# Optimization experiments

Measured on AMD Instinct MI355X. Metric: run time of the kernel, lower is better.

Reference implementation:

```python
import math
import jax, jax.numpy as jnp
import numpy as np

B, T, C, H = 2, 2048, 1024, 16
MAX_SEQ = 2048


def _make_pe(max_seq: int, dim: int, base: float = 10000.0) -> np.ndarray:
    pe = np.zeros((max_seq, dim), dtype=np.float32)
    position = np.arange(max_seq, dtype=np.float32)[:, None]
    div_term = np.exp(np.arange(0, dim, 2, dtype=np.float32) * (-math.log(base) / dim))
    pe[:, 0::2] = np.sin(position * div_term)
    pe[:, 1::2] = np.cos(position * div_term)
    return pe


def setup_inputs() -> dict:
    key = jax.random.key(0)
    k1, k2, k3 = jax.random.split(key, 3)
    x = jax.random.normal(k1, (B, T, C), dtype=jnp.float32)
    # torch Linear default init scale ~ 1/sqrt(fan_in)
    w_qkv = jax.random.normal(k2, (3 * C, C), dtype=jnp.float32) / math.sqrt(C)
    w_proj = jax.random.normal(k3, (C, C), dtype=jnp.float32) / math.sqrt(C)
    pe = jnp.asarray(_make_pe(MAX_SEQ, C))
    return {"x": x, "w_qkv": w_qkv, "w_proj": w_proj, "pe": pe}


def reference(x, w_qkv, w_proj, pe):
    b, t, c = x.shape
    h = H
    d = c // h
    # RoPE module adds sinusoidal PE under torch.no_grad() -> stop_gradient
    xp = jax.lax.stop_gradient(x + pe[None, :t, :])
    qkv = xp @ w_qkv.T  # [b, t, 3c]
    q, k, v = jnp.split(qkv, 3, axis=-1)
    q = q.reshape(b, t, h, d).transpose(0, 2, 1, 3)  # bhtd
    k = k.reshape(b, t, h, d).transpose(0, 2, 1, 3)
    v = v.reshape(b, t, h, d).transpose(0, 2, 1, 3)
    att = jnp.einsum("bhqd,bhkd->bhqk", q, k) * (1.0 / math.sqrt(d))
    causal = jnp.tril(jnp.ones((t, t), dtype=bool))  # [t, t]
    att = jnp.where(causal[None, None], att, -jnp.inf)
    att = jax.nn.softmax(att, axis=-1)
    y = jnp.einsum("bhqk,bhkd->bhqd", att, v)
    y = y.transpose(0, 2, 1, 3).reshape(b, t, c)
    return y @ w_proj.T
```

## Files before the change

kernel.cpp:

```cpp
#include <hip/hip_runtime.h>
#include <cstdint>

typedef __bf16 bf16x8 __attribute__((ext_vector_type(8)));
typedef __bf16 bf16x4 __attribute__((ext_vector_type(4)));
typedef float  f32x4  __attribute__((ext_vector_type(4)));

static constexpr int kB = 2, kT = 2048, kC = 1024, kH = 16, kD = 64;
static constexpr int kK = 1024;

__device__ __forceinline__ uint16_t f2bf(float f) {
  uint32_t u = __builtin_bit_cast(uint32_t, f);
  u += 0x7FFFu + ((u >> 16) & 1u);
  return (uint16_t)(u >> 16);
}

__device__ __forceinline__ void gl_lds16(const void* g, void* l) {
  __builtin_amdgcn_global_load_lds((__attribute__((address_space(1))) void*)(void*)g,
                                   (__attribute__((address_space(3))) void*)l, 16, 0, 0);
}

__device__ const uint8_t kJT[48] = {
    95, 127, 94, 15, 126, 93, 125, 92, 14, 124, 91, 123, 90, 13, 122, 89,
    121, 88, 12, 120, 87, 119, 86, 11, 118, 85, 117, 84, 10, 116, 83, 115,
    82, 9, 114, 81, 113, 80, 8, 112, 7, 6, 5, 4, 3, 2, 1, 0};

__global__ __launch_bounds__(256) void prep_all(const float* __restrict__ x,
                                                const float* __restrict__ pe,
                                                const float* __restrict__ wqkv,
                                                const float* __restrict__ wproj,
                                                uint16_t* __restrict__ xp,
                                                uint16_t* __restrict__ wq,
                                                uint16_t* __restrict__ wp) {
  constexpr int NX = kB * kT * kC / 4;
  constexpr int NWQ = 3 * kC * kC / 4;
  const int i = blockIdx.x * 256 + threadIdx.x;
  if (i < NX) {
    const float4 xv = ((const float4*)x)[i];
    const int c4 = i & (kC / 4 - 1);
    const int t = (i / (kC / 4)) & (kT - 1);
    const float4 pv = ((const float4*)pe)[t * (kC / 4) + c4];
    ushort4 o;
    o.x = f2bf(xv.x + pv.x);
    o.y = f2bf(xv.y + pv.y);
    o.z = f2bf(xv.z + pv.z);
    o.w = f2bf(xv.w + pv.w);
    ((ushort4*)xp)[i] = o;
  } else if (i < NX + NWQ) {
    const int j = i - NX;
    const float4 v = ((const float4*)wqkv)[j];
    ushort4 u;
    u.x = f2bf(v.x); u.y = f2bf(v.y); u.z = f2bf(v.z); u.w = f2bf(v.w);
    ((ushort4*)wq)[j] = u;
  } else {
    const int j = i - NX - NWQ;
    const float4 v = ((const float4*)wproj)[j];
    ushort4 u;
    u.x = f2bf(v.x); u.y = f2bf(v.y); u.z = f2bf(v.z); u.w = f2bf(v.w);
    ((ushort4*)wp)[j] = u;
  }
}

__global__ __launch_bounds__(512, 2) void gemm_qkv(const uint16_t* __restrict__ A,
                                                   const uint16_t* __restrict__ W,
                                                   uint16_t* __restrict__ qb,
                                                   uint16_t* __restrict__ kb,
                                                   uint16_t* __restrict__ vT) {
  __shared__ __align__(1024) char lds[131072];
  const int tid = threadIdx.x;
  const int lane = tid & 63;
  const int wid = tid >> 6;
  const int l15 = lane & 15, l4 = lane >> 4;
  const int WM = wid >> 2, WN = wid & 3;
  const int orig = (int)blockIdx.x;
  const int xcd = orig & 7, j = orig >> 3;
  const int m0 = (xcd * 2 + (j & 1)) * 256;
  const int n0 = (j >> 1) * 256;

  f32x4 acc[2][4][4] = {};
  bf16x8 bfp[2][4];

  auto stage = [&](int isA, int buf, int kt) {
#pragma unroll
    for (int c = 0; c < 4; ++c) {
      const int off = (c * 512 + tid) * 16;
      const int lr = off >> 7, cbl = off & 127;
      const size_t grow = (size_t)((isA ? m0 : n0) + lr) * kK + kt * 64;
      gl_lds16((const char*)(isA ? A : W) + grow * 2 + (cbl ^ ((lr & 7) << 4)),
               lds + (isA ? 0 : 65536) + buf * 32768 + off);
    }
  };

#define QKV_PHASE(CBUF, H, SA, SBUF, KT, VM)                                      \
  {                                                                               \
    stage(SA, SBUF, KT);                                                          \
    if (VM == 4)                                                                  \
      asm volatile("s_waitcnt vmcnt(4)" ::: "memory");                            \
    else                                                                          \
      asm volatile("s_waitcnt vmcnt(8)" ::: "memory");                            \
    __builtin_amdgcn_s_barrier();                                                 \
    asm volatile("" ::: "memory");                                                \
    const char* Ab = lds + (CBUF)*32768;                                          \
    const char* Bb = lds + 65536 + (CBUF)*32768;                                  \
    if ((H) == 0) {                                                               \
      _Pragma("unroll") for (int ks = 0; ks < 2; ++ks)                            \
          _Pragma("unroll") for (int nt = 0; nt < 4; ++nt) {                      \
        const int lr = WN * 64 + nt * 16 + l15;                                   \
        bfp[ks][nt] = *(const bf16x8*)(Bb + lr * 128 +                            \
                                       ((ks * 64 + l4 * 16) ^ ((lr & 7) << 4)));  \
      }                                                                           \
    }                                                                             \
    _Pragma("unroll") for (int ks = 0; ks < 2; ++ks) {                            \
      bf16x8 af[4];                                                               \
      _Pragma("unroll") for (int mt = 0; mt < 4; ++mt) {                          \
        const int lr = (H)*128 + WM * 64 + mt * 16 + l15;                         \
        af[mt] = *(const bf16x8*)(Ab + lr * 128 +                                 \
                                  ((ks * 64 + l4 * 16) ^ ((lr & 7) << 4)));       \
      }                                                                           \
      __builtin_amdgcn_s_setprio(1);                                              \
      _Pragma("unroll") for (int mt = 0; mt < 4; ++mt)                            \
          _Pragma("unroll") for (int nt = 0; nt < 4; ++nt)                        \
              acc[H][mt][nt] = __builtin_amdgcn_mfma_f32_16x16x32_bf16(           \
                  af[mt], bfp[ks][nt], acc[H][mt][nt], 0, 0, 0);                  \
      __builtin_amdgcn_s_setprio(0);                                              \
    }                                                                             \
    asm volatile("" ::: "memory");                                                \
    __builtin_amdgcn_s_barrier();                                                 \
    asm volatile("" ::: "memory");                                                \
  }

  stage(1, 0, 0);
  stage(0, 0, 0);

  for (int i = 0; i < 8; ++i) {
    const int ktb1 = 2 * i + 1;
    const int ktb0 = (2 * i + 2 > 15) ? 15 : 2 * i + 2;
    QKV_PHASE(0, 0, 1, 1, ktb1, 4);
    QKV_PHASE(0, 1, 0, 1, ktb1, 8);
    QKV_PHASE(1, 0, 1, 0, ktb0, 4);
    QKV_PHASE(1, 1, 0, 0, ktb0, 8);
  }
  asm volatile("s_waitcnt vmcnt(0)" ::: "memory");
  __builtin_amdgcn_s_barrier();
  asm volatile("" ::: "memory");

  const int sec = n0 >> 10;
  const int b = m0 >> 11, tb = m0 & (kT - 1);
  if (sec < 2) {
    uint16_t* dst = (sec == 0) ? qb : kb;
#pragma unroll
    for (int h = 0; h < 2; ++h)
#pragma unroll
      for (int mt = 0; mt < 4; ++mt)
#pragma unroll
        for (int nt = 0; nt < 4; ++nt)
#pragma unroll
          for (int r = 0; r < 4; ++r) {
            const int m = h * 128 + WM * 64 + mt * 16 + l4 * 4 + r;
            const int nn = (n0 & (kC - 1)) + WN * 64 + nt * 16 + l15;
            const int hh = nn >> 6, d = nn & 63;
            dst[((size_t)((b * kH + hh) * kT + tb + m)) * kD + d] =
                f2bf(acc[h][mt][nt][r]);
          }
  } else {
#pragma unroll
    for (int h = 0; h < 2; ++h)
#pragma unroll
      for (int mt = 0; mt < 4; ++mt)
#pragma unroll
        for (int nt = 0; nt < 4; ++nt) {
          const int nl = WN * 64 + nt * 16 + l15;
          const int mb2 = (h * 128 + WM * 64 + mt * 16 + l4 * 4) * 2;
          ushort4 pk;
          pk.x = f2bf(acc[h][mt][nt][0]);
          pk.y = f2bf(acc[h][mt][nt][1]);
          pk.z = f2bf(acc[h][mt][nt][2]);
          pk.w = f2bf(acc[h][mt][nt][3]);
          *(ushort4*)(lds + nl * 512 + (mb2 ^ ((nl & 7) << 4))) = pk;
        }
    asm volatile("" ::: "memory");
    __builtin_amdgcn_s_barrier();
    asm volatile("" ::: "memory");
#pragma unroll
    for (int it = 0; it < 16; ++it) {
      const int chunk = it * 512 + tid;
      const int nr = chunk >> 5, mb = (chunk & 31) * 16;
      const bf16x8 v = *(const bf16x8*)(lds + nr * 512 + (mb ^ ((nr & 7) << 4)));
      const int nn = (n0 - 2048) + nr;
      const int hh = nn >> 6, d = nn & 63;
      *(bf16x8*)(vT + ((size_t)((b * kH + hh) * kD + d)) * kT + tb + (chunk & 31) * 8) = v;
    }
  }
#undef QKV_PHASE
}

__global__ __launch_bounds__(256, 2) void gemm_proj(const uint16_t* __restrict__ A,
                                                    const uint16_t* __restrict__ W,
                                                    float* __restrict__ out) {
  __shared__ __align__(1024) char lds[65536];
  const int tid = threadIdx.x;
  const int lane = tid & 63;
  const int wid = tid >> 6;
  const int l15 = lane & 15, l4 = lane >> 4;
  const int WM = wid >> 1, WN = wid & 1;
  const int orig = (int)blockIdx.x;
  const int xcd = orig & 7, j = orig >> 3;
  const int m0 = (xcd * 4 + (j & 3)) * 128;
  const int n0 = (j >> 2) * 128;

  f32x4 acc[2][2][4] = {};
  bf16x8 bfp[2][4];

  auto stage = [&](int isA, int buf, int kt) {
#pragma unroll
    for (int c = 0; c < 4; ++c) {
      const int off = (c * 256 + tid) * 16;
      const int lr = off >> 7, cbl = off & 127;
      const size_t grow = (size_t)((isA ? m0 : n0) + lr) * kK + kt * 64;
      gl_lds16((const char*)(isA ? A : W) + grow * 2 + (cbl ^ ((lr & 7) << 4)),
               lds + (isA ? 0 : 32768) + buf * 16384 + off);
    }
  };

#define PRJ_PHASE(CBUF, H, SA, SBUF, KT, VM)                                      \
  {                                                                               \
    stage(SA, SBUF, KT);                                                          \
    if (VM == 4)                                                                  \
      asm volatile("s_waitcnt vmcnt(4)" ::: "memory");                            \
    else                                                                          \
      asm volatile("s_waitcnt vmcnt(8)" ::: "memory");                            \
    __builtin_amdgcn_s_barrier();                                                 \
    asm volatile("" ::: "memory");                                                \
    const char* Ab = lds + (CBUF)*16384;                                          \
    const char* Bb = lds + 32768 + (CBUF)*16384;                                  \
    if ((H) == 0) {                                                               \
      _Pragma("unroll") for (int ks = 0; ks < 2; ++ks)                            \
          _Pragma("unroll") for (int nt = 0; nt < 4; ++nt) {                      \
        const int lr = WN * 64 + nt * 16 + l15;                                   \
        bfp[ks][nt] = *(const bf16x8*)(Bb + lr * 128 +                            \
                                       ((ks * 64 + l4 * 16) ^ ((lr & 7) << 4)));  \
      }                                                                           \
    }                                                                             \
    _Pragma("unroll") for (int ks = 0; ks < 2; ++ks) {                            \
      bf16x8 af[2];                                                               \
      _Pragma("unroll") for (int mt = 0; mt < 2; ++mt) {                          \
        const int lr = (H)*64 + WM * 32 + mt * 16 + l15;                          \
        af[mt] = *(const bf16x8*)(Ab + lr * 128 +                                 \
                                  ((ks * 64 + l4 * 16) ^ ((lr & 7) << 4)));       \
      }                                                                           \
      __builtin_amdgcn_s_setprio(1);                                              \
      _Pragma("unroll") for (int mt = 0; mt < 2; ++mt)                            \
          _Pragma("unroll") for (int nt = 0; nt < 4; ++nt)                        \
              acc[H][mt][nt] = __builtin_amdgcn_mfma_f32_16x16x32_bf16(           \
                  af[mt], bfp[ks][nt], acc[H][mt][nt], 0, 0, 0);                  \
      __builtin_amdgcn_s_setprio(0);                                              \
    }                                                                             \
    asm volatile("" ::: "memory");                                                \
    __builtin_amdgcn_s_barrier();                                                 \
    asm volatile("" ::: "memory");                                                \
  }

  stage(1, 0, 0);
  stage(0, 0, 0);

  for (int i = 0; i < 8; ++i) {
    const int ktb1 = 2 * i + 1;
    const int ktb0 = (2 * i + 2 > 15) ? 15 : 2 * i + 2;
    PRJ_PHASE(0, 0, 1, 1, ktb1, 4);
    PRJ_PHASE(0, 1, 0, 1, ktb1, 8);
    PRJ_PHASE(1, 0, 1, 0, ktb0, 4);
    PRJ_PHASE(1, 1, 0, 0, ktb0, 8);
  }
  asm volatile("s_waitcnt vmcnt(0)" ::: "memory");
  __builtin_amdgcn_s_barrier();
  asm volatile("" ::: "memory");

#pragma unroll
  for (int h = 0; h < 2; ++h)
#pragma unroll
    for (int mt = 0; mt < 2; ++mt)
#pragma unroll
      for (int nt = 0; nt < 4; ++nt)
#pragma unroll
        for (int r = 0; r < 4; ++r) {
          const int m = m0 + h * 64 + WM * 32 + mt * 16 + l4 * 4 + r;
          const int n = n0 + WN * 64 + nt * 16 + l15;
          out[(size_t)m * kC + n] = acc[h][mt][nt][r];
        }
#undef PRJ_PHASE
}

__global__ __launch_bounds__(256, 4) void attn(const uint16_t* __restrict__ qb,
                                               const uint16_t* __restrict__ kb,
                                               const uint16_t* __restrict__ vT,
                                               uint16_t* __restrict__ y,
                                               uint16_t* __restrict__ opart,
                                               float* __restrict__ ml) {
  __shared__ __align__(1024) char lds[40960];
  const int lane = threadIdx.x & 63;
  const int wid = threadIdx.x >> 6;
  const int l15 = lane & 15, l4 = lane >> 4;
  const int bh = blockIdx.x;
  const int enc = kJT[blockIdx.y];
  const int qt = enc & 31, half = (enc >> 5) & 1, split = enc >> 6;
  const int nkt = qt + 1;
  const int h0 = (nkt + 1) >> 1;
  const int lo = (split && half) ? h0 : 0;
  const int hi = split ? (half ? nkt : h0) : nkt;
  const int q0 = qt * 64 + wid * 16;
  const size_t base = (size_t)bh * kT * kD;
  const uint16_t* Q = qb + base;
  const uint16_t* Kp = kb + base;
  const uint16_t* Vt = vT + base;
  char* P = lds + 32768 + wid * 2048;
  const int xr = (l15 & 7) << 4;

  bf16x8 qf[2];
#pragma unroll
  for (int ks = 0; ks < 2; ++ks) {
    bf16x8 t = *(const bf16x8*)(Q + (size_t)(q0 + l15) * kD + ks * 32 + l4 * 8);
#pragma unroll
    for (int i = 0; i < 8; ++i) t[i] = (__bf16)((float)t[i] * 0.1803368801f);
    qf[ks] = t;
  }
  bf16x8 ones;
#pragma unroll
  for (int i = 0; i < 8; ++i) ones[i] = (__bf16)1.0f;

  float m_ = -1e30f;
  f32x4 o[4];
  f32x4 ol = {0.f, 0.f, 0.f, 0.f};
#pragma unroll
  for (int nt = 0; nt < 4; ++nt) o[nt] = (f32x4){0.f, 0.f, 0.f, 0.f};

  auto STAGE = [&](int bi, int k0) {
#pragma unroll
    for (int c = 0; c < 2; ++c) {
      const int call = wid * 2 + c;
      const int row = call * 8 + (lane >> 3);
      const int colb = (((lane & 7) ^ ((lane >> 3) & 7)) << 4);
      gl_lds16((const char*)Kp + ((size_t)(k0 + row) * kD) * 2 + colb,
               lds + bi * 8192 + call * 1024);
      gl_lds16((const char*)Vt + ((size_t)row * kT + k0) * 2 + colb,
               lds + 16384 + bi * 8192 + call * 1024);
    }
  };

  int cur = 0;
  STAGE(0, lo * 64);
  for (int kt = lo; kt < hi; ++kt) {
    const int k0 = kt * 64;
    asm volatile("s_waitcnt vmcnt(0)" ::: "memory");
    __builtin_amdgcn_s_barrier();
    asm volatile("" ::: "memory");
    if (kt + 1 < hi) STAGE(cur ^ 1, k0 + 64);

    const char* Kb = lds + cur * 8192;
    const char* Vb = lds + 16384 + cur * 8192;

    f32x4 s[4] = {};
    __builtin_amdgcn_s_setprio(1);
#pragma unroll
    for (int ks = 0; ks < 2; ++ks)
#pragma unroll
      for (int nt = 0; nt < 4; ++nt) {
        const bf16x8 kf =
            *(const bf16x8*)(Kb + (nt * 16 + l15) * 128 + ((ks * 64 + l4 * 16) ^ xr));
        s[nt] = __builtin_amdgcn_mfma_f32_16x16x32_bf16(kf, qf[ks], s[nt], 0, 0, 0);
      }
    __builtin_amdgcn_s_setprio(0);

    if (kt == nkt - 1) {
      const int qq = q0 + l15;
#pragma unroll
      for (int nt = 0; nt < 4; ++nt)
#pragma unroll
        for (int r = 0; r < 4; ++r)
          if (k0 + nt * 16 + l4 * 4 + r > qq) s[nt][r] = -1e30f;
    }

    float tmx[4];
#pragma unroll
    for (int nt = 0; nt < 4; ++nt)
      tmx[nt] = fmaxf(fmaxf(fmaxf(s[nt][0], s[nt][1]), s[nt][2]), s[nt][3]);
    const float pm = fmaxf(fmaxf(fmaxf(tmx[0], tmx[1]), tmx[2]), tmx[3]);
    if (!__all(pm <= m_ + 11.0f)) {
      float rm = fmaxf(pm, __shfl_xor(pm, 16));
      rm = fmaxf(rm, __shfl_xor(rm, 32));
      const float newm = fmaxf(m_, rm);
      const float sc = exp2f(m_ - newm);
      m_ = newm;
#pragma unroll
      for (int nt = 0; nt < 4; ++nt)
#pragma unroll
        for (int r = 0; r < 4; ++r) o[nt][r] *= sc;
#pragma unroll
      for (int r = 0; r < 4; ++r) ol[r] *= sc;
    }
#pragma unroll
    for (int nt = 0; nt < 4; ++nt)
#pragma unroll
      for (int r = 0; r < 4; ++r) s[nt][r] = exp2f(s[nt][r] - m_);

#pragma unroll
    for (int nt = 0; nt < 4; ++nt) {
      bf16x4 pk;
#pragma unroll
      for (int r = 0; r < 4; ++r) pk[r] = (__bf16)s[nt][r];
      *(bf16x4*)(P + l15 * 128 + ((nt * 32 + l4 * 8) ^ xr)) = pk;
    }
    asm volatile("s_waitcnt lgkmcnt(0)" ::: "memory");
    __builtin_amdgcn_sched_barrier(0);

    bf16x8 pf[2];
#pragma unroll
    for (int ks = 0; ks < 2; ++ks)
      pf[ks] = *(const bf16x8*)(P + l15 * 128 + ((ks * 64 + l4 * 16) ^ xr));
    __builtin_amdgcn_s_setprio(1);
#pragma unroll
    for (int ks = 0; ks < 2; ++ks) {
#pragma unroll
      for (int nt = 0; nt < 4; ++nt) {
        const bf16x8 vf =
            *(const bf16x8*)(Vb + (nt * 16 + l15) * 128 + ((ks * 64 + l4 * 16) ^ xr));
        o[nt] = __builtin_amdgcn_mfma_f32_16x16x32_bf16(vf, pf[ks], o[nt], 0, 0, 0);
      }
      ol = __builtin_amdgcn_mfma_f32_16x16x32_bf16(ones, pf[ks], ol, 0, 0, 0);
    }
    __builtin_amdgcn_s_setprio(0);

    cur ^= 1;
  }

  if (!split) {
    const float inv = 1.0f / ol[0];
    const int b = bh >> 4, h = bh & 15;
    const int q = q0 + l15;
#pragma unroll
    for (int nt = 0; nt < 4; ++nt) {
      bf16x4 yv;
#pragma unroll
      for (int r = 0; r < 4; ++r) yv[r] = (__bf16)(o[nt][r] * inv);
      *(bf16x4*)(y + ((size_t)(b * kT + q)) * kC + h * kD + nt * 16 + l4 * 4) = yv;
    }
  } else {
    const int prow = (qt - 16) * 64 + wid * 16 + l15;
    uint16_t* op = opart + (((size_t)(half * 32 + bh)) * 1024 + prow) * 64;
#pragma unroll
    for (int nt = 0; nt < 4; ++nt) {
      bf16x4 ov;
#pragma unroll
      for (int r = 0; r < 4; ++r) ov[r] = (__bf16)o[nt][r];
      *(bf16x4*)(op + nt * 16 + l4 * 4) = ov;
    }
    if (l4 == 0) {
      float* mlp = ml + (((size_t)(half * 32 + bh)) * 1024 + prow) * 2;
      mlp[0] = m_;
      mlp[1] = ol[0];
    }
  }
}

__global__ __launch_bounds__(256) void attn_combine(const uint16_t* __restrict__ op,
                                                    const float* __restrict__ ml,
                                                    uint16_t* __restrict__ y) {
  const int gid = blockIdx.x * 256 + threadIdx.x;
  const int r = gid >> 3, c8 = (gid & 7) * 8;
  const int bh = r >> 10, row = r & 1023;
  const float m0 = ml[((size_t)(bh * 1024 + row)) * 2];
  const float l0 = ml[((size_t)(bh * 1024 + row)) * 2 + 1];
  const float m1 = ml[((size_t)((32 + bh) * 1024 + row)) * 2];
  const float l1 = ml[((size_t)((32 + bh) * 1024 + row)) * 2 + 1];
  const float M = fmaxf(m0, m1);
  const float w0 = exp2f(m0 - M), w1 = exp2f(m1 - M);
  const float inv = 1.0f / (l0 * w0 + l1 * w1);
  const bf16x8 a = *(const bf16x8*)(op + ((size_t)(bh * 1024 + row)) * 64 + c8);
  const bf16x8 bvec = *(const bf16x8*)(op + ((size_t)((32 + bh) * 1024 + row)) * 64 + c8);
  const int b = bh >> 4, h = bh & 15;
  const int t = (16 + (row >> 6)) * 64 + (row & 63);
  bf16x8 out;
#pragma unroll
  for (int j = 0; j < 8; ++j)
    out[j] = (__bf16)(((float)a[j] * w0 + (float)bvec[j] * w1) * inv);
  *(bf16x8*)(y + ((size_t)(b * kT + t)) * kC + h * kD + c8) = out;
}

extern "C" void kernel_launch(void* const* d_in, const int* in_sizes, int n_in,
                              void* d_out, int out_size, void* d_ws, size_t ws_size,
                              hipStream_t stream) {
  const float* x = (const float*)d_in[0];
  const float* wqkv = (const float*)d_in[1];
  const float* wproj = (const float*)d_in[2];
  const float* pe = (const float*)d_in[3];

  char* ws = (char*)d_ws;
  uint16_t* xp = (uint16_t*)(ws);
  uint16_t* wq = (uint16_t*)(ws + (size_t)(8u << 20));
  uint16_t* wp = (uint16_t*)(ws + (size_t)(14u << 20));
  uint16_t* qbuf = (uint16_t*)(ws + (size_t)(16u << 20));
  uint16_t* kbuf = (uint16_t*)(ws + (size_t)(24u << 20));
  uint16_t* vTb = (uint16_t*)(ws + (size_t)(32u << 20));
  uint16_t* opart = (uint16_t*)(ws + (size_t)(40u << 20));
  float* mlb = (float*)(ws + (size_t)(48u << 20));

  prep_all<<<dim3(8192), 256, 0, stream>>>(x, pe, wqkv, wproj, xp, wq, wp);

  gemm_qkv<<<dim3(192), 512, 0, stream>>>(xp, wq, qbuf, kbuf, vTb);

  attn<<<dim3(kB * kH, 48), 256, 0, stream>>>(qbuf, kbuf, vTb, xp, opart, mlb);
  attn_combine<<<dim3(1024), 256, 0, stream>>>(opart, mlb, xp);

  gemm_proj<<<dim3(256), 256, 0, stream>>>(xp, wp, (float*)d_out);
}
```

Measured before the change: 102.1 us.

## Split attention KV ranges into up to four chunks by query tile depth

Replaces the two-way split-K scheme for the upper half of query tiles with a graded split: tiles 24-31 use four KV chunks, 16-23 three, 8-15 two, and the rest one. The grid grows from 48 to 80 blocks per head, and the combine kernel now merges up to four partials for rows from query tile 8 onward. The aim is to even out per-block work and give the GPU more parallel blocks, so the long causal tiles no longer dominate the tail. In exchange, more partial outputs go through global memory and the combine kernel handles more rows.

```diff
diff --git a/kernel.cpp b/kernel.cpp
--- a/kernel.cpp
+++ b/kernel.cpp
@@ -18,11 +18,6 @@
   __builtin_amdgcn_global_load_lds((__attribute__((address_space(1))) void*)(void*)g,
                                    (__attribute__((address_space(3))) void*)l, 16, 0, 0);
 }
-
-__device__ const uint8_t kJT[48] = {
-    95, 127, 94, 15, 126, 93, 125, 92, 14, 124, 91, 123, 90, 13, 122, 89,
-    121, 88, 12, 120, 87, 119, 86, 11, 118, 85, 117, 84, 10, 116, 83, 115,
-    82, 9, 114, 81, 113, 80, 8, 112, 7, 6, 5, 4, 3, 2, 1, 0};
 
 __global__ __launch_bounds__(256) void prep_all(const float* __restrict__ x,
                                                 const float* __restrict__ pe,
@@ -300,12 +295,18 @@
   const int wid = threadIdx.x >> 6;
   const int l15 = lane & 15, l4 = lane >> 4;
   const int bh = blockIdx.x;
-  const int enc = kJT[blockIdx.y];
-  const int qt = enc & 31, half = (enc >> 5) & 1, split = enc >> 6;
+  const int jy = (int)blockIdx.y;
+  int qt, c;
+  if (jy < 32) { qt = 31 - (jy >> 2); c = jy & 3; }
+  else if (jy < 56) { const int t = jy - 32; qt = 23 - t / 3; c = t % 3; }
+  else if (jy < 72) { const int t = jy - 56; qt = 15 - ((t) >> 1); c = t & 1; }
+  else { qt = 7 - (jy - 72); c = 0; }
   const int nkt = qt + 1;
-  const int h0 = (nkt + 1) >> 1;
-  const int lo = (split && half) ? h0 : 0;
-  const int hi = split ? (half ? nkt : h0) : nkt;
+  const int nch = (qt >= 24) ? 4 : (qt >= 16) ? 3 : (qt >= 8) ? 2 : 1;
+  const int bas = nkt / nch, rem = nkt % nch;
+  const int lo = c * bas + (c < rem ? c : rem);
+  const int hi = lo + bas + (c < rem ? 1 : 0);
+  const int split = (nch > 1);
   const int q0 = qt * 64 + wid * 16;
   const size_t base = (size_t)bh * kT * kD;
   const uint16_t* Q = qb + base;
@@ -334,8 +335,8 @@
 
   auto STAGE = [&](int bi, int k0) {
 #pragma unroll
-    for (int c = 0; c < 2; ++c) {
-      const int call = wid * 2 + c;
+    for (int cc = 0; cc < 2; ++cc) {
+      const int call = wid * 2 + cc;
       const int row = call * 8 + (lane >> 3);
       const int colb = (((lane & 7) ^ ((lane >> 3) & 7)) << 4);
       gl_lds16((const char*)Kp + ((size_t)(k0 + row) * kD) * 2 + colb,
@@ -443,8 +444,11 @@
       *(bf16x4*)(y + ((size_t)(b * kT + q)) * kC + h * kD + nt * 16 + l4 * 4) = yv;
     }
   } else {
-    const int prow = (qt - 16) * 64 + wid * 16 + l15;
-    uint16_t* op = opart + (((size_t)(half * 32 + bh)) * 1024 + prow) * 64;
+    const int slot = (qt >= 24) ? ((qt - 24) * 4 + c)
+                   : (qt >= 16) ? (32 + (qt - 16) * 3 + c)
+                                : (56 + (qt - 8) * 2 + c);
+    const int row64 = wid * 16 + l15;
+    uint16_t* op = opart + (((size_t)(bh * 72 + slot)) * 64 + row64) * 64;
 #pragma unroll
     for (int nt = 0; nt < 4; ++nt) {
       bf16x4 ov;
@@ -453,7 +457,7 @@
       *(bf16x4*)(op + nt * 16 + l4 * 4) = ov;
     }
     if (l4 == 0) {
-      float* mlp = ml + (((size_t)(half * 32 + bh)) * 1024 + prow) * 2;
+      float* mlp = ml + (((size_t)(bh * 72 + slot)) * 64 + row64) * 2;
       mlp[0] = m_;
       mlp[1] = ol[0];
     }
@@ -465,22 +469,47 @@
                                                     uint16_t* __restrict__ y) {
   const int gid = blockIdx.x * 256 + threadIdx.x;
   const int r = gid >> 3, c8 = (gid & 7) * 8;
-  const int bh = r >> 10, row = r & 1023;
-  const float m0 = ml[((size_t)(bh * 1024 + row)) * 2];
-  const float l0 = ml[((size_t)(bh * 1024 + row)) * 2 + 1];
-  const float m1 = ml[((size_t)((32 + bh) * 1024 + row)) * 2];
-  const float l1 = ml[((size_t)((32 + bh) * 1024 + row)) * 2 + 1];
-  const float M = fmaxf(m0, m1);
-  const float w0 = exp2f(m0 - M), w1 = exp2f(m1 - M);
-  const float inv = 1.0f / (l0 * w0 + l1 * w1);
-  const bf16x8 a = *(const bf16x8*)(op + ((size_t)(bh * 1024 + row)) * 64 + c8);
-  const bf16x8 bvec = *(const bf16x8*)(op + ((size_t)((32 + bh) * 1024 + row)) * 64 + c8);
+  const int bh = r / 1536, rowg = r % 1536;
+  const int qt = 8 + (rowg >> 6), row64 = rowg & 63;
+  int s0, nch;
+  if (qt >= 24) { s0 = (qt - 24) * 4; nch = 4; }
+  else if (qt >= 16) { s0 = 32 + (qt - 16) * 3; nch = 3; }
+  else { s0 = 56 + (qt - 8) * 2; nch = 2; }
+  float mv[4], lv[4];
+#pragma unroll
+  for (int i = 0; i < 4; ++i) {
+    if (i < nch) {
+      const size_t mi = (((size_t)(bh * 72 + s0 + i)) * 64 + row64) * 2;
+      mv[i] = ml[mi];
+      lv[i] = ml[mi + 1];
+    } else {
+      mv[i] = -1e30f;
+      lv[i] = 0.f;
+    }
+  }
+  const float M = fmaxf(fmaxf(mv[0], mv[1]), fmaxf(mv[2], mv[3]));
+  float w[4], L = 0.f;
+#pragma unroll
+  for (int i = 0; i < 4; ++i) {
+    w[i] = exp2f(mv[i] - M);
+    L += lv[i] * w[i];
+  }
+  float acc[8] = {};
+#pragma unroll
+  for (int i = 0; i < 4; ++i) {
+    if (i < nch) {
+      const bf16x8 ov =
+          *(const bf16x8*)(op + (((size_t)(bh * 72 + s0 + i)) * 64 + row64) * 64 + c8);
+#pragma unroll
+      for (int jj = 0; jj < 8; ++jj) acc[jj] += (float)ov[jj] * w[i];
+    }
+  }
+  const float inv = 1.0f / L;
   const int b = bh >> 4, h = bh & 15;
-  const int t = (16 + (row >> 6)) * 64 + (row & 63);
+  const int t = 512 + rowg;
   bf16x8 out;
 #pragma unroll
-  for (int j = 0; j < 8; ++j)
-    out[j] = (__bf16)(((float)a[j] * w0 + (float)bvec[j] * w1) * inv);
+  for (int jj = 0; jj < 8; ++jj) out[jj] = (__bf16)(acc[jj] * inv);
   *(bf16x8*)(y + ((size_t)(b * kT + t)) * kC + h * kD + c8) = out;
 }
 
@@ -500,14 +529,14 @@
   uint16_t* kbuf = (uint16_t*)(ws + (size_t)(24u << 20));
   uint16_t* vTb = (uint16_t*)(ws + (size_t)(32u << 20));
   uint16_t* opart = (uint16_t*)(ws + (size_t)(40u << 20));
-  float* mlb = (float*)(ws + (size_t)(48u << 20));
+  float* mlb = (float*)(ws + (size_t)(60u << 20));
 
   prep_all<<<dim3(8192), 256, 0, stream>>>(x, pe, wqkv, wproj, xp, wq, wp);
 
   gemm_qkv<<<dim3(192), 512, 0, stream>>>(xp, wq, qbuf, kbuf, vTb);
 
-  attn<<<dim3(kB * kH, 48), 256, 0, stream>>>(qbuf, kbuf, vTb, xp, opart, mlb);
-  attn_combine<<<dim3(1024), 256, 0, stream>>>(opart, mlb, xp);
+  attn<<<dim3(kB * kH, 80), 256, 0, stream>>>(qbuf, kbuf, vTb, xp, opart, mlb);
+  attn_combine<<<dim3(1536), 256, 0, stream>>>(opart, mlb, xp);
 
   gemm_proj<<<dim3(256), 256, 0, stream>>>(xp, wp, (float*)d_out);
 }
```

Result: slower. 107.1 us (+4.9%).
